# Performance work log

Measured on AMD Instinct MI355X. Metric: run time of the kernel, lower is better.

## Reference

```python
import jax, jax.numpy as jnp
import numpy as np

PRE, POST, BATCH, HIST = 1024, 1024, 256, 50
CONN_PROB = 0.1

def setup_inputs() -> dict:
    key = jax.random.key(0)
    k1, k2, k3, k4, k5 = jax.random.split(key, 5)
    pre_spikes = (jax.random.uniform(k1, (BATCH, PRE)) < 0.2).astype(jnp.float32)   # sparse spike trains
    post_spikes = (jax.random.uniform(k2, (BATCH, POST)) < 0.2).astype(jnp.float32)
    connectivity_mask = (jax.random.uniform(k3, (PRE, POST)) < CONN_PROB).astype(jnp.float32)
    synaptic_weights = jax.random.normal(k4, (PRE, POST), dtype=jnp.float32) * 0.1 * connectivity_mask
    correlation_history = jax.random.normal(k5, (PRE, POST, HIST), dtype=jnp.float32) * 0.01
    return {
        "pre_spikes": pre_spikes,
        "post_spikes": post_spikes,
        "synaptic_weights": synaptic_weights,
        "connectivity_mask": connectivity_mask,
        "correlation_history": correlation_history,
        "pre_activity": jnp.zeros((PRE,), jnp.float32),
        "post_activity": jnp.zeros((POST,), jnp.float32),
        "corr_index": 7,
    }

def reference(pre_spikes, post_spikes, synaptic_weights, connectivity_mask,
              correlation_history, pre_activity, post_activity, corr_index):
    # EMA of population activity (buffer updates in the torch module)
    pre_mean = pre_spikes.mean(axis=0)    # [pre]
    post_mean = post_spikes.mean(axis=0)  # [post]
    new_pre_activity = 0.99 * pre_activity + 0.01 * pre_mean
    new_post_activity = 0.99 * post_activity + 0.01 * post_mean

    # circular-buffer scatter: write current outer-product correlation at slot idx
    idx = corr_index % correlation_history.shape[-1]
    current_correlation = jnp.outer(pre_mean, post_mean)            # [pre, post]
    new_history = correlation_history.at[:, :, idx].set(current_correlation)

    # masked matmul: fuse elementwise mask into the GEMM operand
    effective_weights = synaptic_weights * connectivity_mask        # [pre, post]
    synaptic_current = pre_spikes @ effective_weights               # [batch, post]

    # connectivity_info['average_correlation'] (plasticity disabled: current_time <= 1.0)
    average_correlation = new_history.mean(axis=-1)                 # [pre, post]

    return (synaptic_current, new_pre_activity, new_post_activity,
            average_correlation, new_history)
```

## Files before the change

### kernel.cpp

```cpp
#include <hip/hip_runtime.h>

#define PRE   1024
#define POST  1024
#define BATCH 256
#define HIST  50
#define NPAIR (PRE * POST)

typedef float nf4 __attribute__((ext_vector_type(4)));

#define MCOLS 16
#define GBM 64
#define GBN 64
#define GBK 16
#define GKSPLIT 8
#define GLD 68

__global__ __launch_bounds__(256) void fusedA_kernel(
    const float* __restrict__ pre_spikes,
    const float* __restrict__ post_spikes,
    const float* __restrict__ pre_activity,
    const float* __restrict__ post_activity,
    float* __restrict__ ws_means,
    float* __restrict__ out_pre_act,
    float* __restrict__ out_post_act,
    const float* __restrict__ W,
    const float* __restrict__ Mk,
    float* __restrict__ C,
    float* __restrict__ Cpart,
    int use_part)
{
    int tid = threadIdx.x;

    if (blockIdx.x < 128) {
        __shared__ float red[256];
        int blk = blockIdx.x;
        bool is_pre = blk < 64;
        const float* mat = is_pre ? pre_spikes : post_spikes;
        const float* act = is_pre ? pre_activity : post_activity;
        float* out_act   = is_pre ? out_pre_act : out_post_act;
        float* ws        = is_pre ? ws_means : ws_means + PRE;
        int col0 = (blk & 63) * MCOLS;

        int col = col0 + (tid & 15);
        int chunk = tid >> 4;
        float s = 0.f;
#pragma unroll
        for (int r = chunk * 16; r < chunk * 16 + 16; ++r)
            s += mat[r * 1024 + col];
        red[tid] = s;
        __syncthreads();
        if (tid < 16) {
            float t = 0.f;
#pragma unroll
            for (int k = 0; k < 16; ++k)
                t += red[k * 16 + tid];
            float m = t * (1.0f / BATCH);
            int c = col0 + tid;
            ws[c] = m;
            out_act[c] = 0.99f * act[c] + 0.01f * m;
        }
        return;
    }

    __shared__ __align__(16) float As[GBK * GLD];
    __shared__ __align__(16) float Bs[GBK * GLD];
    int id = blockIdx.x - 128;
    int bn = id & 15;
    int bm = (id >> 4) & 3;
    int bz = id >> 6;
    int kbase = bz * (PRE / GKSPLIT);

    int ar = tid >> 2;
    int ak = (tid & 3) << 2;
    int bk = tid >> 4;
    int bn4 = (tid & 15) << 2;
    int tn4 = (tid & 15) << 2;
    int tm4 = (tid >> 4) << 2;

    const float* Ap = &pre_spikes[(bm * GBM + ar) * PRE + kbase + ak];
    const float* Wp = &W [(size_t)(kbase + bk) * POST + bn * GBN + bn4];
    const float* Mp = &Mk[(size_t)(kbase + bk) * POST + bn * GBN + bn4];

    float acc[4][4] = {};

    for (int k0 = 0; k0 < PRE / GKSPLIT; k0 += GBK) {
        float4 av = *(const float4*)(Ap + k0);
        float4 wv = *(const float4*)(Wp + (size_t)k0 * POST);
        float4 mv = *(const float4*)(Mp + (size_t)k0 * POST);
        wv.x *= mv.x; wv.y *= mv.y; wv.z *= mv.z; wv.w *= mv.w;
        __syncthreads();
        As[(ak + 0) * GLD + ar] = av.x;
        As[(ak + 1) * GLD + ar] = av.y;
        As[(ak + 2) * GLD + ar] = av.z;
        As[(ak + 3) * GLD + ar] = av.w;
        *(float4*)&Bs[bk * GLD + bn4] = wv;
        __syncthreads();
#pragma unroll
        for (int kk = 0; kk < GBK; ++kk) {
            float4 a4 = *(const float4*)&As[kk * GLD + tm4];
            float4 b4 = *(const float4*)&Bs[kk * GLD + tn4];
            const float* ap = (const float*)&a4;
            const float* bp = (const float*)&b4;
#pragma unroll
            for (int i = 0; i < 4; ++i)
#pragma unroll
                for (int j = 0; j < 4; ++j)
                    acc[i][j] += ap[i] * bp[j];
        }
    }
    if (use_part) {
        float* dst = &Cpart[(size_t)bz * (BATCH * POST)
                            + (size_t)(bm * GBM + tm4) * POST + bn * GBN + tn4];
#pragma unroll
        for (int i = 0; i < 4; ++i) {
            float4 r; r.x = acc[i][0]; r.y = acc[i][1]; r.z = acc[i][2]; r.w = acc[i][3];
            *(float4*)(dst + (size_t)i * POST) = r;
        }
    } else {
#pragma unroll
        for (int i = 0; i < 4; ++i)
#pragma unroll
            for (int j = 0; j < 4; ++j)
                atomicAdd(&C[(size_t)(bm * GBM + tm4 + i) * POST + bn * GBN + tn4 + j],
                          acc[i][j]);
    }
}

#define PPB 128
#define HTHREADS 320
#define NIT 5
#define NRED 205

__global__ __launch_bounds__(HTHREADS) void fusedB_kernel(
    const float* __restrict__ hist_in,
    const int*   __restrict__ corr_index,
    const float* __restrict__ ws_means,
    float* __restrict__ hist_out,
    float* __restrict__ avg_out,
    const float* __restrict__ Cpart,
    float* __restrict__ C,
    int nred)
{
    int tid = threadIdx.x;

    if ((int)blockIdx.x < nred) {
        int g = blockIdx.x * HTHREADS + tid;
        if (g < BATCH * POST / 4) {
            const nf4* p4 = (const nf4*)Cpart;
            nf4 s = p4[g];
#pragma unroll
            for (int z = 1; z < GKSPLIT; ++z)
                s += p4[(size_t)z * (BATCH * POST / 4) + g];
            ((nf4*)C)[g] = s;
        }
        return;
    }

    __shared__ __align__(16) float tile[PPB * HIST + 2];
    int p0 = (blockIdx.x - nred) * PPB;
    int idx = ((corr_index[0] % HIST) + HIST) % HIST;

    const nf4* in4   = (const nf4*)(hist_in + (size_t)p0 * HIST);
    nf4*       out4  = (nf4*)(hist_out + (size_t)p0 * HIST);
    nf4*       tile4 = (nf4*)tile;

    nf4 v[NIT];
#pragma unroll
    for (int it = 0; it < NIT; ++it)
        v[it] = __builtin_nontemporal_load(&in4[it * HTHREADS + tid]);

#pragma unroll
    for (int it = 0; it < NIT; ++it) {
        int fl = it * HTHREADS + tid;
        int r0 = 4 * fl;
        int pl = r0 / HIST;
        int t0 = r0 - pl * HIST;
        int d  = idx - t0;
        int d2 = idx + HIST - t0;
        bool needA = ((unsigned)d) < 4u;
        bool needB = (d2 < 4);
        float corr = 0.f;
        if (needA | needB) {
            int pair = needA ? (p0 + pl) : (p0 + pl + 1);
            corr = ws_means[pair >> 10] * ws_means[PRE + (pair & (POST - 1))];
        }
        nf4 w = v[it];
        w.x = (d == 0) ? corr : w.x;
        w.y = (d == 1) ? corr : w.y;
        w.z = (d == 2 || d2 == 2) ? corr : w.z;
        w.w = (d == 3 || d2 == 3) ? corr : w.w;
        v[it] = w;
        tile4[fl] = w;
    }
    __syncthreads();

#pragma unroll
    for (int it = 0; it < NIT; ++it)
        __builtin_nontemporal_store(v[it], &out4[it * HTHREADS + tid]);

    if (tid < 2 * PPB) {
        int pl   = tid >> 1;
        int half = tid & 1;
        const float2* tp = (const float2*)&tile[pl * HIST];
        float s = 0.f;
#pragma unroll
        for (int k = 0; k < 13; ++k) {
            int f2 = 2 * k + half;
            float2 w = tp[f2];
            if (f2 < 25) s += w.x + w.y;
        }
        s += __shfl_xor(s, 1);
        if (half == 0)
            __builtin_nontemporal_store(s * (1.0f / HIST), &avg_out[p0 + pl]);
    }
}

extern "C" void kernel_launch(void* const* d_in, const int* in_sizes, int n_in,
                              void* d_out, int out_size, void* d_ws, size_t ws_size,
                              hipStream_t stream)
{
    const float* pre_spikes  = (const float*)d_in[0];
    const float* post_spikes = (const float*)d_in[1];
    const float* W           = (const float*)d_in[2];
    const float* Mk          = (const float*)d_in[3];
    const float* hist        = (const float*)d_in[4];
    const float* pre_act     = (const float*)d_in[5];
    const float* post_act    = (const float*)d_in[6];
    const int*   corr_index  = (const int*)d_in[7];

    float* out = (float*)d_out;
    float* out_current  = out;
    float* out_pre_act  = out + 262144;
    float* out_post_act = out + 263168;
    float* out_avg      = out + 264192;
    float* out_hist     = out + 1312768;

    float* ws_means = (float*)d_ws;
    float* cpart    = ws_means + 4096;
    size_t ws_need  = (size_t)4096 * 4 + (size_t)GKSPLIT * BATCH * POST * 4;
    int use_part    = ws_size >= ws_need;

    if (!use_part)
        (void)hipMemsetAsync(out_current, 0, (size_t)BATCH * POST * sizeof(float), stream);

    fusedA_kernel<<<128 + 512, 256, 0, stream>>>(
        pre_spikes, post_spikes, pre_act, post_act,
        ws_means, out_pre_act, out_post_act,
        W, Mk, out_current, cpart, use_part);

    int nred = use_part ? NRED : 0;
    fusedB_kernel<<<nred + NPAIR / PPB, HTHREADS, 0, stream>>>(
        hist, corr_index, ws_means, out_hist, out_avg,
        cpart, out_current, nred);
}
```

Before: 370.4 us.

## Rewrite history update to per-pair thread pairs without shared memory tile

Replaces the history kernel's coalesced float4 loads, shared-memory tile and barrier with a scheme where two threads own each (pre,post) pair. Each thread loads interleaved float2 chunks of its pair's 50-entry history, patches the current slot in registers, stores it back and reduces via a shuffle. This removes the LDS staging and the __syncthreads, but adds strided 8-byte accesses with a 200-byte stride between lanes. The history stores also drop their nontemporal hint, and the block size goes from 320 to 256 threads.

```diff
diff --git a/kernel.cpp b/kernel.cpp
--- a/kernel.cpp
+++ b/kernel.cpp
@@ -7,6 +7,7 @@
 #define NPAIR (PRE * POST)
 
 typedef float nf4 __attribute__((ext_vector_type(4)));
+typedef float nf2 __attribute__((ext_vector_type(2)));
 
 #define MCOLS 16
 #define GBM 64
@@ -126,12 +127,10 @@
     }
 }
 
-#define PPB 128
-#define HTHREADS 320
-#define NIT 5
-#define NRED 205
-
-__global__ __launch_bounds__(HTHREADS) void fusedB_kernel(
+#define HPB 128
+#define NRED 256
+
+__global__ __launch_bounds__(256) void fusedB_kernel(
     const float* __restrict__ hist_in,
     const int*   __restrict__ corr_index,
     const float* __restrict__ ws_means,
@@ -144,75 +143,55 @@
     int tid = threadIdx.x;
 
     if ((int)blockIdx.x < nred) {
-        int g = blockIdx.x * HTHREADS + tid;
-        if (g < BATCH * POST / 4) {
-            const nf4* p4 = (const nf4*)Cpart;
-            nf4 s = p4[g];
-#pragma unroll
-            for (int z = 1; z < GKSPLIT; ++z)
-                s += p4[(size_t)z * (BATCH * POST / 4) + g];
-            ((nf4*)C)[g] = s;
-        }
+        int g = blockIdx.x * 256 + tid;
+        const nf4* p4 = (const nf4*)Cpart;
+        nf4 s = p4[g];
+#pragma unroll
+        for (int z = 1; z < GKSPLIT; ++z)
+            s += p4[(size_t)z * (BATCH * POST / 4) + g];
+        ((nf4*)C)[g] = s;
         return;
     }
 
-    __shared__ __align__(16) float tile[PPB * HIST + 2];
-    int p0 = (blockIdx.x - nred) * PPB;
+    int b  = (int)blockIdx.x - nred;
+    int pl = tid >> 1;
+    int h  = tid & 1;
+    int p  = b * HPB + pl;
     int idx = ((corr_index[0] % HIST) + HIST) % HIST;
 
-    const nf4* in4   = (const nf4*)(hist_in + (size_t)p0 * HIST);
-    nf4*       out4  = (nf4*)(hist_out + (size_t)p0 * HIST);
-    nf4*       tile4 = (nf4*)tile;
-
-    nf4 v[NIT];
-#pragma unroll
-    for (int it = 0; it < NIT; ++it)
-        v[it] = __builtin_nontemporal_load(&in4[it * HTHREADS + tid]);
-
-#pragma unroll
-    for (int it = 0; it < NIT; ++it) {
-        int fl = it * HTHREADS + tid;
-        int r0 = 4 * fl;
-        int pl = r0 / HIST;
-        int t0 = r0 - pl * HIST;
-        int d  = idx - t0;
-        int d2 = idx + HIST - t0;
-        bool needA = ((unsigned)d) < 4u;
-        bool needB = (d2 < 4);
-        float corr = 0.f;
-        if (needA | needB) {
-            int pair = needA ? (p0 + pl) : (p0 + pl + 1);
-            corr = ws_means[pair >> 10] * ws_means[PRE + (pair & (POST - 1))];
-        }
-        nf4 w = v[it];
-        w.x = (d == 0) ? corr : w.x;
-        w.y = (d == 1) ? corr : w.y;
-        w.z = (d == 2 || d2 == 2) ? corr : w.z;
-        w.w = (d == 3 || d2 == 3) ? corr : w.w;
-        v[it] = w;
-        tile4[fl] = w;
-    }
-    __syncthreads();
-
-#pragma unroll
-    for (int it = 0; it < NIT; ++it)
-        __builtin_nontemporal_store(v[it], &out4[it * HTHREADS + tid]);
-
-    if (tid < 2 * PPB) {
-        int pl   = tid >> 1;
-        int half = tid & 1;
-        const float2* tp = (const float2*)&tile[pl * HIST];
-        float s = 0.f;
-#pragma unroll
-        for (int k = 0; k < 13; ++k) {
-            int f2 = 2 * k + half;
-            float2 w = tp[f2];
-            if (f2 < 25) s += w.x + w.y;
-        }
-        s += __shfl_xor(s, 1);
-        if (half == 0)
-            __builtin_nontemporal_store(s * (1.0f / HIST), &avg_out[p0 + pl]);
-    }
+    const float* ibase = hist_in  + (size_t)p * HIST + 2 * h;
+    float*       obase = hist_out + (size_t)p * HIST + 2 * h;
+    int nk = 13 - h;
+
+    nf2 v[13];
+#pragma unroll
+    for (int k = 0; k < 13; ++k)
+        if (k < nk)
+            v[k] = __builtin_nontemporal_load((const nf2*)(ibase + 4 * k));
+
+    float corr = ws_means[p >> 10] * ws_means[PRE + (p & (POST - 1))];
+    bool hm  = (h == ((idx >> 1) & 1));
+    int kidx = idx >> 2;
+    int comp = idx & 1;
+#pragma unroll
+    for (int k = 0; k < 13; ++k)
+        if (k < nk) {
+            bool m = hm && (k == kidx);
+            v[k].x = (m && comp == 0) ? corr : v[k].x;
+            v[k].y = (m && comp == 1) ? corr : v[k].y;
+        }
+
+    float s = 0.f;
+#pragma unroll
+    for (int k = 0; k < 13; ++k)
+        if (k < nk) {
+            *(nf2*)(obase + 4 * k) = v[k];
+            s += v[k].x + v[k].y;
+        }
+
+    s += __shfl_xor(s, 1);
+    if (h == 0)
+        avg_out[p] = s * (1.0f / HIST);
 }
 
 extern "C" void kernel_launch(void* const* d_in, const int* in_sizes, int n_in,
@@ -249,7 +228,7 @@
         W, Mk, out_current, cpart, use_part);
 
     int nred = use_part ? NRED : 0;
-    fusedB_kernel<<<nred + NPAIR / PPB, HTHREADS, 0, stream>>>(
+    fusedB_kernel<<<nred + NPAIR / HPB, 256, 0, stream>>>(
         hist, corr_index, ws_means, out_hist, out_avg,
         cpart, out_current, nred);
 }
```

Result: slower. 478.1 us (+29.1%).
